# Performance work log

Hardware: AMD Instinct MI355X
Metric: run time of the kernel (lower is better)

Reference implementation:

```python
import jax, jax.numpy as jnp
import numpy as np

S, H, F = 8192, 1024, 15
IN = 1 + F  # scalar target + features per timestep


def _uniform(key, shape, k):
    return jax.random.uniform(key, shape, jnp.float32, -k, k)


def setup_inputs() -> dict:
    key = jax.random.key(0)
    ks = jax.random.split(key, 16)
    k_lstm = 1.0 / np.sqrt(H)  # torch nn.LSTM init scale
    k_ffn = 1.0 / np.sqrt(H)
    return {
        "x": jax.random.normal(ks[0], (S,), jnp.float32),
        "mask": jax.random.randint(ks[1], (S,), 0, 2, jnp.int32),
        "features": jax.random.normal(ks[2], (S, F), jnp.float32),
        "teacher_force_ratio": 1,
        "w_ih0": _uniform(ks[3], (4 * H, IN), k_lstm),
        "w_hh0": _uniform(ks[4], (4 * H, H), k_lstm),
        "b_ih0": _uniform(ks[5], (4 * H,), k_lstm),
        "b_hh0": _uniform(ks[6], (4 * H,), k_lstm),
        "w_ih1": _uniform(ks[7], (4 * H, H), k_lstm),
        "w_hh1": _uniform(ks[8], (4 * H, H), k_lstm),
        "b_ih1": _uniform(ks[9], (4 * H,), k_lstm),
        "b_hh1": _uniform(ks[10], (4 * H,), k_lstm),
        "w_ffn": _uniform(ks[11], (1, H), k_ffn),
        "b_ffn": _uniform(ks[12], (1,), k_ffn),
    }


def _lstm_cell(h, c, inp, w_ih, w_hh, b_ih, b_hh):
    # torch gate order: i, f, g, o
    g = inp @ w_ih.T + h @ w_hh.T + b_ih + b_hh  # (4H,)
    i, f, gg, o = jnp.split(g, 4)
    c_new = jax.nn.sigmoid(f) * c + jax.nn.sigmoid(i) * jnp.tanh(gg)
    h_new = jax.nn.sigmoid(o) * jnp.tanh(c_new)
    return h_new, c_new


def reference(x, mask, features, teacher_force_ratio,
              w_ih0, w_hh0, b_ih0, b_hh0,
              w_ih1, w_hh1, b_ih1, b_hh1,
              w_ffn, b_ffn):
    # teacher_force_ratio==1 => feed x[i] whenever mask[i]!=0 (deterministic).
    # Step 0 always feeds x[0].
    tf = jnp.float32(teacher_force_ratio >= 1)
    use_x = jnp.concatenate([jnp.ones((1,), bool),
                             (mask[1:] != 0) & (tf > 0)])

    def step(carry, inputs):
        h0, c0, h1, c1, prev_y = carry
        xi, sel, fi = inputs
        scalar_in = jnp.where(sel, xi, prev_y)
        inp = jnp.concatenate([scalar_in[None], fi])  # (IN,)
        h0, c0 = _lstm_cell(h0, c0, inp, w_ih0, w_hh0, b_ih0, b_hh0)
        h1, c1 = _lstm_cell(h1, c1, h0, w_ih1, w_hh1, b_ih1, b_hh1)
        y = w_ffn[0] @ h1 + b_ffn[0]  # scalar prediction
        return (h0, c0, h1, c1, y), y

    z = jnp.zeros((H,), x.dtype)
    carry0 = (z, z, z, z, jnp.float32(0.0))
    _, y_hat = jax.lax.scan(step, carry0, (x, use_x, features))
    return y_hat  # (S,)
```

## Files before the change

### kernel.cpp

```cpp
#include <hip/hip_runtime.h>
#include <stdint.h>

typedef float f32x4 __attribute__((ext_vector_type(4)));

#define SLEN 8192
#define NBLK 256

#define RING_PAR 8192
#define H0_OFF   16384
#define WS_BYTES 32768

__device__ __forceinline__ void st_chunk(void* addr, f32x4 v) {
  asm volatile("global_store_dwordx4 %0, %1, off sc0 sc1"
               :: "v"(addr), "v"(v) : "memory");
}
__device__ __forceinline__ f32x4 ld_chunk(const void* a) {
  f32x4 v;
  asm volatile("global_load_dwordx4 %0, %1, off sc0 sc1\n\ts_waitcnt vmcnt(0)"
               : "=v"(v) : "v"(a) : "memory");
  return v;
}
__device__ __forceinline__ void ld2(const void* a, f32x4& v0, f32x4& v1) {
  asm volatile("global_load_dwordx4 %0, %2, off sc0 sc1\n\t"
               "global_load_dwordx4 %1, %2, off offset:16 sc0 sc1\n\t"
               "s_waitcnt vmcnt(0)"
               : "=v"(v0), "=v"(v1) : "v"(a) : "memory");
}
__device__ __forceinline__ void poll2(const void* a, unsigned tag, f32x4& v0, f32x4& v1) {
  ld2(a, v0, v1);
  while (__float_as_uint(v0.w) != tag || __float_as_uint(v1.w) != tag) {
    __builtin_amdgcn_s_sleep(1);
    ld2(a, v0, v1);
  }
}
__device__ __forceinline__ f32x4 poll1(const void* a, unsigned tag) {
  f32x4 v = ld_chunk(a);
  while (__float_as_uint(v.w) != tag) {
    __builtin_amdgcn_s_sleep(1);
    v = ld_chunk(a);
  }
  return v;
}

__device__ __forceinline__ float sigm(float v) { return 1.f / (1.f + expf(-v)); }
__device__ __forceinline__ float tanh_f(float v) {
  float e = expf(-2.f * fabsf(v));
  return copysignf((1.f - e) / (1.f + e), v);
}
__device__ __forceinline__ float lstm_h(float a0, float a1, float a2, float a3, float& c) {
  float ii = sigm(a0), ff = sigm(a1), gg = tanh_f(a2), oo = sigm(a3);
  c = ff * c + ii * gg;
  return oo * tanh_f(c);
}

__device__ __forceinline__ float dpp_red(float x) {
  x += __int_as_float(__builtin_amdgcn_update_dpp(0, __float_as_int(x), 0x111, 0xf, 0xf, true));
  x += __int_as_float(__builtin_amdgcn_update_dpp(0, __float_as_int(x), 0x112, 0xf, 0xf, true));
  x += __int_as_float(__builtin_amdgcn_update_dpp(0, __float_as_int(x), 0x114, 0xf, 0xf, true));
  x += __int_as_float(__builtin_amdgcn_update_dpp(0, __float_as_int(x), 0x118, 0xf, 0xf, true));
  x += __int_as_float(__builtin_amdgcn_update_dpp(0, __float_as_int(x), 0x142, 0xa, 0xf, true));
  x += __int_as_float(__builtin_amdgcn_update_dpp(0, __float_as_int(x), 0x143, 0xc, 0xf, true));
  return x;
}
__device__ __forceinline__ float dot4(f32x4 a, f32x4 b) {
  return a.x * b.x + a.y * b.y + a.z * b.z + a.w * b.w;
}
__device__ __forceinline__ int lds_idx4(int j) { return (j >> 2) * 20 + (j & 3) * 4; }

__global__ __launch_bounds__(512, 2) void lstm_fused(
    const float* __restrict__ x, const int* __restrict__ mask,
    const float* __restrict__ feat, const int* __restrict__ tfp,
    const float* __restrict__ w_ih0, const float* __restrict__ w_hh0,
    const float* __restrict__ b_ih0, const float* __restrict__ b_hh0,
    const float* __restrict__ w_ih1, const float* __restrict__ w_hh1,
    const float* __restrict__ b_ih1, const float* __restrict__ b_hh1,
    const float* __restrict__ w_ffn, const float* __restrict__ b_ffn,
    float* __restrict__ out, char* __restrict__ ws)
{
  char* h1ring = ws;
  char* h0ring = ws + H0_OFF;
  const int tid = threadIdx.x, lane = tid & 63, wv = tid >> 6;
  const int blk = blockIdx.x;
  const int u = wv & 3;
  const int m = blk * 4 + u;
  const bool L1w = wv < 4;

  __shared__ __align__(16) float wh1_lds[16 * 1280];
  __shared__ __align__(16) float lh0[1280];
  __shared__ __align__(16) float lh1[1280];
  __shared__ float lyp[256];
  __shared__ float g1h[4], g1yp[4], g0h[4];
  __shared__ float lys;

  f32x4 W[4][4];
  {
    const float* Wsrc = L1w ? w_ih1 : w_hh0;
#pragma unroll
    for (int g = 0; g < 4; ++g) {
      const f32x4* s = reinterpret_cast<const f32x4*>(
          Wsrc + (size_t)(1024 * g + m) * 1024 + lane * 16);
#pragma unroll
      for (int q = 0; q < 4; ++q) W[g][q] = s[q];
    }
  }
  float wA[4], wB[4];
#pragma unroll
  for (int g = 0; g < 4; ++g) {
    const int r = 1024 * g + m;
    if (L1w) {
      wA[g] = (lane == 16) ? (b_ih1[r] + b_hh1[r]) : 0.f;
      wB[g] = 0.f;
    } else {
      wA[g] = (lane < 16) ? w_ih0[r * 16 + lane]
            : (lane == 16 ? (b_ih0[r] + b_hh0[r]) : 0.f);
      wB[g] = w_ih0[r * 16];
    }
  }
  const float wffn = w_ffn[m];
  const float bf = b_ffn[0];
  float cc = 0.f;

  for (int ch = tid; ch < 1024; ch += 512) {
    const int r = ch >> 6, kc = ch & 63;
    const int grow = 1024 * (r & 3) + blk * 4 + (r >> 2);
    const f32x4* src = reinterpret_cast<const f32x4*>(
        w_hh1 + (size_t)grow * 1024 + kc * 16);
    f32x4* dst = reinterpret_cast<f32x4*>(&wh1_lds[r * 1280 + kc * 20]);
    dst[0] = src[0]; dst[1] = src[1]; dst[2] = src[2]; dst[3] = src[3];
  }
  __syncthreads();

  const bool tf1 = (*tfp) >= 1;

  for (int t = 0; t < SLEN; ++t) {
    const bool use_x = (t == 0) || (tf1 && mask[t] != 0);
    const bool needy = (t > 0) && !use_x;
    float acc0[4];

    if (L1w) {
      if (t > 0) {
        __builtin_amdgcn_s_setprio(1);
        float a[4];
        const f32x4* h0v = reinterpret_cast<const f32x4*>(&lh0[lane * 20]);
        f32x4 p0 = h0v[0], p1 = h0v[1], p2 = h0v[2], p3 = h0v[3];
#pragma unroll
        for (int g = 0; g < 4; ++g)
          a[g] = wA[g] + dot4(W[g][0], p0) + dot4(W[g][1], p1) +
                          dot4(W[g][2], p2) + dot4(W[g][3], p3);
        if (t > 1) {
          const f32x4* h1v = reinterpret_cast<const f32x4*>(&lh1[lane * 20]);
          f32x4 q0 = h1v[0], q1 = h1v[1], q2 = h1v[2], q3 = h1v[3];
#pragma unroll
          for (int g = 0; g < 4; ++g) {
            const f32x4* wb = reinterpret_cast<const f32x4*>(
                &wh1_lds[(u * 4 + g) * 1280 + lane * 20]);
            a[g] += dot4(wb[0], q0) + dot4(wb[1], q1) +
                    dot4(wb[2], q2) + dot4(wb[3], q3);
          }
        }
#pragma unroll
        for (int g = 0; g < 4; ++g) a[g] = dpp_red(a[g]);
        if (lane == 63) {
          float h = lstm_h(a[0], a[1], a[2], a[3], cc);
          g1h[u] = h; g1yp[u] = wffn * h;
        }
        __builtin_amdgcn_s_setprio(0);
      }
    } else {
      float base = (lane == 0) ? (use_x ? x[t] : 0.f)
                 : (lane < 16) ? feat[t * 15 + lane - 1]
                 : (lane == 16) ? 1.f : 0.f;
#pragma unroll
      for (int g = 0; g < 4; ++g) acc0[g] = wA[g] * base;
      if (t > 0) {
        const f32x4* h0v = reinterpret_cast<const f32x4*>(&lh0[lane * 20]);
        f32x4 p0 = h0v[0], p1 = h0v[1], p2 = h0v[2], p3 = h0v[3];
#pragma unroll
        for (int g = 0; g < 4; ++g)
          acc0[g] += dot4(W[g][0], p0) + dot4(W[g][1], p1) +
                     dot4(W[g][2], p2) + dot4(W[g][3], p3);
      }
#pragma unroll
      for (int g = 0; g < 4; ++g) acc0[g] = dpp_red(acc0[g]);
      if (blk == 0 && wv == 4 && t >= 2 && (tf1 && mask[t - 1] != 0)) {
        float s = (lyp[lane * 4] + lyp[lane * 4 + 1]) +
                  (lyp[lane * 4 + 2] + lyp[lane * 4 + 3]);
        s = dpp_red(s);
        if (lane == 63) out[t - 2] = s + bf;
      }
    }
    __syncthreads();

    if (t > 0 && tid < 2) {
      f32x4 v;
      if (tid == 0) { v.x = g1h[0]; v.y = g1h[1]; v.z = g1h[2]; }
      else { v.x = g1h[3]; v.y = (g1yp[0] + g1yp[1]) + (g1yp[2] + g1yp[3]); v.z = 0.f; }
      v.w = __uint_as_float((unsigned)(t - 1));
      st_chunk(h1ring + ((t - 1) & 1) * RING_PAR + blk * 32 + tid * 16, v);
    }
    if (needy) {
      if (tid < 256) {
        f32x4 v = poll1(h1ring + ((t - 1) & 1) * RING_PAR + tid * 32 + 16,
                        (unsigned)(t - 1));
        lyp[tid] = v.y;
      }
      __syncthreads();
      if (wv == 0) {
        float s = (lyp[lane * 4] + lyp[lane * 4 + 1]) +
                  (lyp[lane * 4 + 2] + lyp[lane * 4 + 3]);
        s = dpp_red(s);
        if (lane == 63) {
          float yy = s + bf;
          lys = yy;
          if (blk == 0) out[t - 1] = yy;
        }
      }
      __syncthreads();
    }
    if (!L1w && lane == 63) {
      __builtin_amdgcn_s_setprio(1);
      if (needy) {
        float yy = lys;
#pragma unroll
        for (int g = 0; g < 4; ++g) acc0[g] += yy * wB[g];
      }
      float h = lstm_h(acc0[0], acc0[1], acc0[2], acc0[3], cc);
      g0h[u] = h;
      __builtin_amdgcn_s_setprio(0);
    }
    __syncthreads();

    if (tid < 2) {
      f32x4 v;
      if (tid == 0) { v.x = g0h[0]; v.y = g0h[1]; v.z = g0h[2]; }
      else { v.x = g0h[3]; v.y = 0.f; v.z = 0.f; }
      v.w = __uint_as_float((unsigned)t);
      st_chunk(h0ring + (t & 1) * RING_PAR + blk * 32 + tid * 16, v);
    }
    if (L1w) {
      if (t > 0) {
        f32x4 v0, v1;
        poll2(h1ring + ((t - 1) & 1) * RING_PAR + tid * 32, (unsigned)(t - 1), v0, v1);
        f32x4 hv; hv.x = v0.x; hv.y = v0.y; hv.z = v0.z; hv.w = v1.x;
        *reinterpret_cast<f32x4*>(&lh1[lds_idx4(tid)]) = hv;
        lyp[tid] = v1.y;
      }
    } else {
      const int j = tid - 256;
      f32x4 v0, v1;
      poll2(h0ring + (t & 1) * RING_PAR + j * 32, (unsigned)t, v0, v1);
      f32x4 hv; hv.x = v0.x; hv.y = v0.y; hv.z = v0.z; hv.w = v1.x;
      *reinterpret_cast<f32x4*>(&lh0[lds_idx4(j)]) = hv;
    }
    __syncthreads();
  }

  if (blk == 0 && wv == 4 && (tf1 && mask[SLEN - 1] != 0)) {
    float s = (lyp[lane * 4] + lyp[lane * 4 + 1]) +
              (lyp[lane * 4 + 2] + lyp[lane * 4 + 3]);
    s = dpp_red(s);
    if (lane == 63) out[SLEN - 2] = s + bf;
  }
  if (L1w) {
    float a[4];
    const f32x4* h0v = reinterpret_cast<const f32x4*>(&lh0[lane * 20]);
    f32x4 p0 = h0v[0], p1 = h0v[1], p2 = h0v[2], p3 = h0v[3];
#pragma unroll
    for (int g = 0; g < 4; ++g)
      a[g] = wA[g] + dot4(W[g][0], p0) + dot4(W[g][1], p1) +
                      dot4(W[g][2], p2) + dot4(W[g][3], p3);
    {
      const f32x4* h1v = reinterpret_cast<const f32x4*>(&lh1[lane * 20]);
      f32x4 q0 = h1v[0], q1 = h1v[1], q2 = h1v[2], q3 = h1v[3];
#pragma unroll
      for (int g = 0; g < 4; ++g) {
        const f32x4* wb = reinterpret_cast<const f32x4*>(
            &wh1_lds[(u * 4 + g) * 1280 + lane * 20]);
        a[g] += dot4(wb[0], q0) + dot4(wb[1], q1) +
                dot4(wb[2], q2) + dot4(wb[3], q3);
      }
    }
#pragma unroll
    for (int g = 0; g < 4; ++g) a[g] = dpp_red(a[g]);
    if (lane == 63) {
      float h = lstm_h(a[0], a[1], a[2], a[3], cc);
      g1h[u] = h; g1yp[u] = wffn * h;
    }
  }
  __syncthreads();
  if (tid < 2) {
    f32x4 v;
    if (tid == 0) { v.x = g1h[0]; v.y = g1h[1]; v.z = g1h[2]; }
    else { v.x = g1h[3]; v.y = (g1yp[0] + g1yp[1]) + (g1yp[2] + g1yp[3]); v.z = 0.f; }
    v.w = __uint_as_float((unsigned)(SLEN - 1));
    st_chunk(h1ring + ((SLEN - 1) & 1) * RING_PAR + blk * 32 + tid * 16, v);
    asm volatile("s_waitcnt vmcnt(0)" ::: "memory");
  }
  if (blk == 0) {
    if (tid < 256) {
      f32x4 v = poll1(h1ring + ((SLEN - 1) & 1) * RING_PAR + tid * 32 + 16,
                      (unsigned)(SLEN - 1));
      lyp[tid] = v.y;
    }
    __syncthreads();
    if (wv == 0) {
      float s = (lyp[lane * 4] + lyp[lane * 4 + 1]) +
                (lyp[lane * 4 + 2] + lyp[lane * 4 + 3]);
      s = dpp_red(s);
      if (lane == 63) out[SLEN - 1] = s + bf;
    }
  }
}

extern "C" void kernel_launch(void* const* d_in, const int* in_sizes, int n_in,
                              void* d_out, int out_size, void* d_ws, size_t ws_size,
                              hipStream_t stream) {
  (void)in_sizes; (void)n_in; (void)out_size; (void)ws_size;
  const float* x      = (const float*)d_in[0];
  const int*   mask   = (const int*)  d_in[1];
  const float* feat   = (const float*)d_in[2];
  const int*   tfp    = (const int*)  d_in[3];
  const float* w_ih0  = (const float*)d_in[4];
  const float* w_hh0  = (const float*)d_in[5];
  const float* b_ih0  = (const float*)d_in[6];
  const float* b_hh0  = (const float*)d_in[7];
  const float* w_ih1  = (const float*)d_in[8];
  const float* w_hh1  = (const float*)d_in[9];
  const float* b_ih1  = (const float*)d_in[10];
  const float* b_hh1  = (const float*)d_in[11];
  const float* w_ffn  = (const float*)d_in[12];
  const float* b_ffn  = (const float*)d_in[13];
  float* out = (float*)d_out;
  char*  ws  = (char*)d_ws;

  hipMemsetAsync(d_ws, 0xFF, (size_t)WS_BYTES, stream);

  lstm_fused<<<dim3(NBLK), dim3(512), 0, stream>>>(
      x, mask, feat, tfp, w_ih0, w_hh0, b_ih0, b_hh0,
      w_ih1, w_hh1, b_ih1, b_hh1, w_ffn, b_ffn, out, ws);
}
```

Baseline: 41.07 ms.

## Publish per-unit hidden states directly with tagged 8-byte stores, drop block syncs

Each lane-63 thread now writes its own h value plus step tag as an 8-byte store into a per-unit slot, instead of gathering into shared memory, syncing, and having two threads write 16-byte chunks. This removes two or three __syncthreads per timestep and one LDS round trip on the critical path. The FFN output dot is computed by every block after polling h1 (redundantly), instead of being packed into the ring by producers. Pollers now check four tags per 32-byte read, and the extra redundant polling and FFN work add load on the interconnect.

Measured after the change: 65.79 ms. +60.2%, slower.

```diff
diff --git a/kernel.cpp b/kernel.cpp
--- a/kernel.cpp
+++ b/kernel.cpp
@@ -2,58 +2,48 @@
 #include <stdint.h>
 
 typedef float f32x4 __attribute__((ext_vector_type(4)));
+typedef unsigned int u32x2 __attribute__((ext_vector_type(2)));
 
 #define SLEN 8192
 #define NBLK 256
 
-#define RING_PAR 8192
-#define H0_OFF   16384
+#define H0E_OFF  16384
 #define WS_BYTES 32768
 
-__device__ __forceinline__ void st_chunk(void* addr, f32x4 v) {
-  asm volatile("global_store_dwordx4 %0, %1, off sc0 sc1"
-               :: "v"(addr), "v"(v) : "memory");
-}
-__device__ __forceinline__ f32x4 ld_chunk(const void* a) {
-  f32x4 v;
-  asm volatile("global_load_dwordx4 %0, %1, off sc0 sc1\n\ts_waitcnt vmcnt(0)"
-               : "=v"(v) : "v"(a) : "memory");
-  return v;
-}
-__device__ __forceinline__ void ld2(const void* a, f32x4& v0, f32x4& v1) {
+static __device__ __forceinline__ void st8(void* addr, float h, unsigned tag) {
+  u32x2 e; e.x = __float_as_uint(h); e.y = tag;
+  asm volatile("global_store_dwordx2 %0, %1, off sc0 sc1"
+               :: "v"(addr), "v"(e) : "memory");
+}
+static __device__ __forceinline__ void ld2(const void* a, f32x4& v0, f32x4& v1) {
   asm volatile("global_load_dwordx4 %0, %2, off sc0 sc1\n\t"
                "global_load_dwordx4 %1, %2, off offset:16 sc0 sc1\n\t"
                "s_waitcnt vmcnt(0)"
                : "=v"(v0), "=v"(v1) : "v"(a) : "memory");
 }
-__device__ __forceinline__ void poll2(const void* a, unsigned tag, f32x4& v0, f32x4& v1) {
+static __device__ __forceinline__ void poll_slot(const void* a, unsigned tag,
+                                                 f32x4& v0, f32x4& v1) {
   ld2(a, v0, v1);
-  while (__float_as_uint(v0.w) != tag || __float_as_uint(v1.w) != tag) {
+  while (__float_as_uint(v0.y) != tag || __float_as_uint(v0.w) != tag ||
+         __float_as_uint(v1.y) != tag || __float_as_uint(v1.w) != tag) {
     __builtin_amdgcn_s_sleep(1);
     ld2(a, v0, v1);
   }
 }
-__device__ __forceinline__ f32x4 poll1(const void* a, unsigned tag) {
-  f32x4 v = ld_chunk(a);
-  while (__float_as_uint(v.w) != tag) {
-    __builtin_amdgcn_s_sleep(1);
-    v = ld_chunk(a);
-  }
-  return v;
-}
-
-__device__ __forceinline__ float sigm(float v) { return 1.f / (1.f + expf(-v)); }
-__device__ __forceinline__ float tanh_f(float v) {
+
+static __device__ __forceinline__ float sigm(float v) { return 1.f / (1.f + expf(-v)); }
+static __device__ __forceinline__ float tanh_f(float v) {
   float e = expf(-2.f * fabsf(v));
   return copysignf((1.f - e) / (1.f + e), v);
 }
-__device__ __forceinline__ float lstm_h(float a0, float a1, float a2, float a3, float& c) {
+static __device__ __forceinline__ float lstm_h(float a0, float a1, float a2, float a3,
+                                               float& c) {
   float ii = sigm(a0), ff = sigm(a1), gg = tanh_f(a2), oo = sigm(a3);
   c = ff * c + ii * gg;
   return oo * tanh_f(c);
 }
 
-__device__ __forceinline__ float dpp_red(float x) {
+static __device__ __forceinline__ float dpp_red(float x) {
   x += __int_as_float(__builtin_amdgcn_update_dpp(0, __float_as_int(x), 0x111, 0xf, 0xf, true));
   x += __int_as_float(__builtin_amdgcn_update_dpp(0, __float_as_int(x), 0x112, 0xf, 0xf, true));
   x += __int_as_float(__builtin_amdgcn_update_dpp(0, __float_as_int(x), 0x114, 0xf, 0xf, true));
@@ -62,10 +52,10 @@
   x += __int_as_float(__builtin_amdgcn_update_dpp(0, __float_as_int(x), 0x143, 0xc, 0xf, true));
   return x;
 }
-__device__ __forceinline__ float dot4(f32x4 a, f32x4 b) {
+static __device__ __forceinline__ float dot4(f32x4 a, f32x4 b) {
   return a.x * b.x + a.y * b.y + a.z * b.z + a.w * b.w;
 }
-__device__ __forceinline__ int lds_idx4(int j) { return (j >> 2) * 20 + (j & 3) * 4; }
+static __device__ __forceinline__ int lds_idx4(int j) { return (j >> 2) * 20 + (j & 3) * 4; }
 
 __global__ __launch_bounds__(512, 2) void lstm_fused(
     const float* __restrict__ x, const int* __restrict__ mask,
@@ -77,20 +67,20 @@
     const float* __restrict__ w_ffn, const float* __restrict__ b_ffn,
     float* __restrict__ out, char* __restrict__ ws)
 {
-  char* h1ring = ws;
-  char* h0ring = ws + H0_OFF;
+  char* h1e = ws;
+  char* h0e = ws + H0E_OFF;
   const int tid = threadIdx.x, lane = tid & 63, wv = tid >> 6;
   const int blk = blockIdx.x;
   const int u = wv & 3;
   const int m = blk * 4 + u;
   const bool L1w = wv < 4;
+  const int j = tid & 255;
 
   __shared__ __align__(16) float wh1_lds[16 * 1280];
   __shared__ __align__(16) float lh0[1280];
   __shared__ __align__(16) float lh1[1280];
-  __shared__ float lyp[256];
-  __shared__ float g1h[4], g1yp[4], g0h[4];
-  __shared__ float lys;
+  __shared__ __align__(16) float lyp[256];
+  __shared__ __align__(16) float lypf[256];
 
   f32x4 W[4][4];
   {
@@ -116,7 +106,8 @@
       wB[g] = w_ih0[r * 16];
     }
   }
-  const float wffn = w_ffn[m];
+  const f32x4 wffn4 = L1w ? reinterpret_cast<const f32x4*>(w_ffn)[j]
+                          : f32x4{0.f, 0.f, 0.f, 0.f};
   const float bf = b_ffn[0];
   float cc = 0.f;
 
@@ -131,11 +122,11 @@
   __syncthreads();
 
   const bool tf1 = (*tfp) >= 1;
+  float acc0[4];
 
   for (int t = 0; t < SLEN; ++t) {
     const bool use_x = (t == 0) || (tf1 && mask[t] != 0);
     const bool needy = (t > 0) && !use_x;
-    float acc0[4];
 
     if (L1w) {
       if (t > 0) {
@@ -162,9 +153,21 @@
         for (int g = 0; g < 4; ++g) a[g] = dpp_red(a[g]);
         if (lane == 63) {
           float h = lstm_h(a[0], a[1], a[2], a[3], cc);
-          g1h[u] = h; g1yp[u] = wffn * h;
+          st8(h1e + ((t - 1) & 1) * 8192 + m * 8, h, (unsigned)(t - 1));
         }
         __builtin_amdgcn_s_setprio(0);
+      }
+      if (needy) {
+        f32x4 v0, v1;
+        poll_slot(h1e + ((t - 1) & 1) * 8192 + j * 32, (unsigned)(t - 1), v0, v1);
+        f32x4 h4; h4.x = v0.x; h4.y = v0.z; h4.z = v1.x; h4.w = v1.z;
+        lypf[j] = dot4(wffn4, h4);
+      }
+      if (blk == 0 && wv == 0 && t >= 2) {
+        f32x4 q = reinterpret_cast<const f32x4*>(lyp)[lane];
+        float s = (q.x + q.y) + (q.z + q.w);
+        s = dpp_red(s);
+        if (lane == 63) out[t - 2] = s + bf;
       }
     } else {
       float base = (lane == 0) ? (use_x ? x[t] : 0.f)
@@ -182,85 +185,44 @@
       }
 #pragma unroll
       for (int g = 0; g < 4; ++g) acc0[g] = dpp_red(acc0[g]);
-      if (blk == 0 && wv == 4 && t >= 2 && (tf1 && mask[t - 1] != 0)) {
-        float s = (lyp[lane * 4] + lyp[lane * 4 + 1]) +
-                  (lyp[lane * 4 + 2] + lyp[lane * 4 + 3]);
+    }
+    __syncthreads();
+
+    if (!L1w) {
+      float y = 0.f;
+      if (needy) {
+        f32x4 q = reinterpret_cast<const f32x4*>(lypf)[lane];
+        float s = (q.x + q.y) + (q.z + q.w);
         s = dpp_red(s);
-        if (lane == 63) out[t - 2] = s + bf;
-      }
-    }
-    __syncthreads();
-
-    if (t > 0 && tid < 2) {
-      f32x4 v;
-      if (tid == 0) { v.x = g1h[0]; v.y = g1h[1]; v.z = g1h[2]; }
-      else { v.x = g1h[3]; v.y = (g1yp[0] + g1yp[1]) + (g1yp[2] + g1yp[3]); v.z = 0.f; }
-      v.w = __uint_as_float((unsigned)(t - 1));
-      st_chunk(h1ring + ((t - 1) & 1) * RING_PAR + blk * 32 + tid * 16, v);
-    }
-    if (needy) {
-      if (tid < 256) {
-        f32x4 v = poll1(h1ring + ((t - 1) & 1) * RING_PAR + tid * 32 + 16,
-                        (unsigned)(t - 1));
-        lyp[tid] = v.y;
-      }
-      __syncthreads();
-      if (wv == 0) {
-        float s = (lyp[lane * 4] + lyp[lane * 4 + 1]) +
-                  (lyp[lane * 4 + 2] + lyp[lane * 4 + 3]);
-        s = dpp_red(s);
-        if (lane == 63) {
-          float yy = s + bf;
-          lys = yy;
-          if (blk == 0) out[t - 1] = yy;
+        y = s + bf;
+      }
+      if (lane == 63) {
+        if (needy) {
+#pragma unroll
+          for (int g = 0; g < 4; ++g) acc0[g] += y * wB[g];
         }
-      }
-      __syncthreads();
-    }
-    if (!L1w && lane == 63) {
-      __builtin_amdgcn_s_setprio(1);
-      if (needy) {
-        float yy = lys;
-#pragma unroll
-        for (int g = 0; g < 4; ++g) acc0[g] += yy * wB[g];
-      }
-      float h = lstm_h(acc0[0], acc0[1], acc0[2], acc0[3], cc);
-      g0h[u] = h;
-      __builtin_amdgcn_s_setprio(0);
-    }
-    __syncthreads();
-
-    if (tid < 2) {
-      f32x4 v;
-      if (tid == 0) { v.x = g0h[0]; v.y = g0h[1]; v.z = g0h[2]; }
-      else { v.x = g0h[3]; v.y = 0.f; v.z = 0.f; }
-      v.w = __uint_as_float((unsigned)t);
-      st_chunk(h0ring + (t & 1) * RING_PAR + blk * 32 + tid * 16, v);
-    }
+        float h = lstm_h(acc0[0], acc0[1], acc0[2], acc0[3], cc);
+        st8(h0e + (t & 1) * 8192 + m * 8, h, (unsigned)t);
+      }
+    }
+
     if (L1w) {
       if (t > 0) {
         f32x4 v0, v1;
-        poll2(h1ring + ((t - 1) & 1) * RING_PAR + tid * 32, (unsigned)(t - 1), v0, v1);
-        f32x4 hv; hv.x = v0.x; hv.y = v0.y; hv.z = v0.z; hv.w = v1.x;
-        *reinterpret_cast<f32x4*>(&lh1[lds_idx4(tid)]) = hv;
-        lyp[tid] = v1.y;
+        poll_slot(h1e + ((t - 1) & 1) * 8192 + j * 32, (unsigned)(t - 1), v0, v1);
+        f32x4 h4; h4.x = v0.x; h4.y = v0.z; h4.z = v1.x; h4.w = v1.z;
+        *reinterpret_cast<f32x4*>(&lh1[lds_idx4(j)]) = h4;
+        lyp[j] = dot4(wffn4, h4);
       }
     } else {
-      const int j = tid - 256;
       f32x4 v0, v1;
-      poll2(h0ring + (t & 1) * RING_PAR + j * 32, (unsigned)t, v0, v1);
-      f32x4 hv; hv.x = v0.x; hv.y = v0.y; hv.z = v0.z; hv.w = v1.x;
-      *reinterpret_cast<f32x4*>(&lh0[lds_idx4(j)]) = hv;
+      poll_slot(h0e + (t & 1) * 8192 + j * 32, (unsigned)t, v0, v1);
+      f32x4 h4; h4.x = v0.x; h4.y = v0.z; h4.z = v1.x; h4.w = v1.z;
+      *reinterpret_cast<f32x4*>(&lh0[lds_idx4(j)]) = h4;
     }
     __syncthreads();
   }
 
-  if (blk == 0 && wv == 4 && (tf1 && mask[SLEN - 1] != 0)) {
-    float s = (lyp[lane * 4] + lyp[lane * 4 + 1]) +
-              (lyp[lane * 4 + 2] + lyp[lane * 4 + 3]);
-    s = dpp_red(s);
-    if (lane == 63) out[SLEN - 2] = s + bf;
-  }
   if (L1w) {
     float a[4];
     const f32x4* h0v = reinterpret_cast<const f32x4*>(&lh0[lane * 20]);
@@ -284,28 +246,28 @@
     for (int g = 0; g < 4; ++g) a[g] = dpp_red(a[g]);
     if (lane == 63) {
       float h = lstm_h(a[0], a[1], a[2], a[3], cc);
-      g1h[u] = h; g1yp[u] = wffn * h;
-    }
-  }
-  __syncthreads();
-  if (tid < 2) {
-    f32x4 v;
-    if (tid == 0) { v.x = g1h[0]; v.y = g1h[1]; v.z = g1h[2]; }
-    else { v.x = g1h[3]; v.y = (g1yp[0] + g1yp[1]) + (g1yp[2] + g1yp[3]); v.z = 0.f; }
-    v.w = __uint_as_float((unsigned)(SLEN - 1));
-    st_chunk(h1ring + ((SLEN - 1) & 1) * RING_PAR + blk * 32 + tid * 16, v);
-    asm volatile("s_waitcnt vmcnt(0)" ::: "memory");
-  }
+      st8(h1e + ((SLEN - 1) & 1) * 8192 + m * 8, h, (unsigned)(SLEN - 1));
+    }
+  }
+  asm volatile("s_waitcnt vmcnt(0)" ::: "memory");
+
   if (blk == 0) {
-    if (tid < 256) {
-      f32x4 v = poll1(h1ring + ((SLEN - 1) & 1) * RING_PAR + tid * 32 + 16,
-                      (unsigned)(SLEN - 1));
-      lyp[tid] = v.y;
+    if (wv == 0) {
+      f32x4 q = reinterpret_cast<const f32x4*>(lyp)[lane];
+      float s = (q.x + q.y) + (q.z + q.w);
+      s = dpp_red(s);
+      if (lane == 63) out[SLEN - 2] = s + bf;
+    }
+    if (L1w) {
+      f32x4 v0, v1;
+      poll_slot(h1e + ((SLEN - 1) & 1) * 8192 + j * 32, (unsigned)(SLEN - 1), v0, v1);
+      f32x4 h4; h4.x = v0.x; h4.y = v0.z; h4.z = v1.x; h4.w = v1.z;
+      lypf[j] = dot4(wffn4, h4);
     }
     __syncthreads();
     if (wv == 0) {
-      float s = (lyp[lane * 4] + lyp[lane * 4 + 1]) +
-                (lyp[lane * 4 + 2] + lyp[lane * 4 + 3]);
+      f32x4 q = reinterpret_cast<const f32x4*>(lypf)[lane];
+      float s = (q.x + q.y) + (q.z + q.w);
       s = dpp_red(s);
       if (lane == 63) out[SLEN - 1] = s + bf;
     }
```

## Remove extra block barriers on feedback path and split ring polling across waves

Applied to the files above, without the earlier changes.

The feedback prediction y for non-teacher-forced steps is now computed by each layer-0 wave itself, which polls the h1 ring directly, instead of going through a poll, a syncthreads, a reduction, a second syncthreads and a shared-memory broadcast. The h1 ring reads are duplicated across both wave halves, and each thread now computes the FFN partial from h1 itself. The h0 ring read is split so every thread polls one 16-byte chunk. This is meant to take two block barriers off the serial per-step critical path, at the cost of more redundant global polling traffic.

Result: slower. 51.76 ms (+26.0%).

```diff
diff --git a/kernel.cpp b/kernel.cpp
--- a/kernel.cpp
+++ b/kernel.cpp
@@ -10,50 +10,74 @@
 #define H0_OFF   16384
 #define WS_BYTES 32768
 
-__device__ __forceinline__ void st_chunk(void* addr, f32x4 v) {
+static __device__ __forceinline__ void st_chunk(void* addr, f32x4 v) {
   asm volatile("global_store_dwordx4 %0, %1, off sc0 sc1"
                :: "v"(addr), "v"(v) : "memory");
 }
-__device__ __forceinline__ f32x4 ld_chunk(const void* a) {
+static __device__ __forceinline__ f32x4 ld16(const void* a) {
   f32x4 v;
   asm volatile("global_load_dwordx4 %0, %1, off sc0 sc1\n\ts_waitcnt vmcnt(0)"
                : "=v"(v) : "v"(a) : "memory");
   return v;
 }
-__device__ __forceinline__ void ld2(const void* a, f32x4& v0, f32x4& v1) {
+static __device__ __forceinline__ f32x4 poll16(const void* a, unsigned tag) {
+  f32x4 v = ld16(a);
+  while (__float_as_uint(v.w) != tag) {
+    __builtin_amdgcn_s_sleep(2);
+    v = ld16(a);
+  }
+  return v;
+}
+static __device__ __forceinline__ void ld32(const void* a, f32x4& v0, f32x4& v1) {
   asm volatile("global_load_dwordx4 %0, %2, off sc0 sc1\n\t"
                "global_load_dwordx4 %1, %2, off offset:16 sc0 sc1\n\t"
                "s_waitcnt vmcnt(0)"
                : "=v"(v0), "=v"(v1) : "v"(a) : "memory");
 }
-__device__ __forceinline__ void poll2(const void* a, unsigned tag, f32x4& v0, f32x4& v1) {
-  ld2(a, v0, v1);
+static __device__ __forceinline__ void poll32(const void* a, unsigned tag,
+                                              f32x4& v0, f32x4& v1) {
+  ld32(a, v0, v1);
   while (__float_as_uint(v0.w) != tag || __float_as_uint(v1.w) != tag) {
-    __builtin_amdgcn_s_sleep(1);
-    ld2(a, v0, v1);
-  }
-}
-__device__ __forceinline__ f32x4 poll1(const void* a, unsigned tag) {
-  f32x4 v = ld_chunk(a);
-  while (__float_as_uint(v.w) != tag) {
-    __builtin_amdgcn_s_sleep(1);
-    v = ld_chunk(a);
-  }
-  return v;
-}
-
-__device__ __forceinline__ float sigm(float v) { return 1.f / (1.f + expf(-v)); }
-__device__ __forceinline__ float tanh_f(float v) {
+    __builtin_amdgcn_s_sleep(2);
+    ld32(a, v0, v1);
+  }
+}
+static __device__ __forceinline__ void ld_y4(const char* a0, const char* a1,
+                                             f32x4& v0, f32x4& v1, f32x4& v2, f32x4& v3) {
+  asm volatile("global_load_dwordx4 %0, %4, off sc0 sc1\n\t"
+               "global_load_dwordx4 %1, %4, off offset:2048 sc0 sc1\n\t"
+               "global_load_dwordx4 %2, %5, off sc0 sc1\n\t"
+               "global_load_dwordx4 %3, %5, off offset:2048 sc0 sc1\n\t"
+               "s_waitcnt vmcnt(0)"
+               : "=v"(v0), "=v"(v1), "=v"(v2), "=v"(v3)
+               : "v"(a0), "v"(a1) : "memory");
+}
+static __device__ __forceinline__ float poll_y4(const char* base, int lane, unsigned tag) {
+  const char* a0 = base + lane * 32 + 16;
+  const char* a1 = a0 + 4096;
+  f32x4 v0, v1, v2, v3;
+  ld_y4(a0, a1, v0, v1, v2, v3);
+  while (__float_as_uint(v0.w) != tag || __float_as_uint(v1.w) != tag ||
+         __float_as_uint(v2.w) != tag || __float_as_uint(v3.w) != tag) {
+    __builtin_amdgcn_s_sleep(2);
+    ld_y4(a0, a1, v0, v1, v2, v3);
+  }
+  return (v0.y + v1.y) + (v2.y + v3.y);
+}
+
+static __device__ __forceinline__ float sigm(float v) { return 1.f / (1.f + expf(-v)); }
+static __device__ __forceinline__ float tanh_f(float v) {
   float e = expf(-2.f * fabsf(v));
   return copysignf((1.f - e) / (1.f + e), v);
 }
-__device__ __forceinline__ float lstm_h(float a0, float a1, float a2, float a3, float& c) {
+static __device__ __forceinline__ float lstm_h(float a0, float a1, float a2, float a3,
+                                               float& c) {
   float ii = sigm(a0), ff = sigm(a1), gg = tanh_f(a2), oo = sigm(a3);
   c = ff * c + ii * gg;
   return oo * tanh_f(c);
 }
 
-__device__ __forceinline__ float dpp_red(float x) {
+static __device__ __forceinline__ float dpp_red(float x) {
   x += __int_as_float(__builtin_amdgcn_update_dpp(0, __float_as_int(x), 0x111, 0xf, 0xf, true));
   x += __int_as_float(__builtin_amdgcn_update_dpp(0, __float_as_int(x), 0x112, 0xf, 0xf, true));
   x += __int_as_float(__builtin_amdgcn_update_dpp(0, __float_as_int(x), 0x114, 0xf, 0xf, true));
@@ -62,10 +86,10 @@
   x += __int_as_float(__builtin_amdgcn_update_dpp(0, __float_as_int(x), 0x143, 0xc, 0xf, true));
   return x;
 }
-__device__ __forceinline__ float dot4(f32x4 a, f32x4 b) {
+static __device__ __forceinline__ float dot4(f32x4 a, f32x4 b) {
   return a.x * b.x + a.y * b.y + a.z * b.z + a.w * b.w;
 }
-__device__ __forceinline__ int lds_idx4(int j) { return (j >> 2) * 20 + (j & 3) * 4; }
+static __device__ __forceinline__ int lds_idx4(int j) { return (j >> 2) * 20 + (j & 3) * 4; }
 
 __global__ __launch_bounds__(512, 2) void lstm_fused(
     const float* __restrict__ x, const int* __restrict__ mask,
@@ -88,9 +112,8 @@
   __shared__ __align__(16) float wh1_lds[16 * 1280];
   __shared__ __align__(16) float lh0[1280];
   __shared__ __align__(16) float lh1[1280];
-  __shared__ float lyp[256];
+  __shared__ __align__(16) float lyp[256];
   __shared__ float g1h[4], g1yp[4], g0h[4];
-  __shared__ float lys;
 
   f32x4 W[4][4];
   {
@@ -116,7 +139,9 @@
       wB[g] = w_ih0[r * 16];
     }
   }
-  const float wffn = w_ffn[m];
+  const float wffn_m = w_ffn[m];
+  const f32x4 wffn4 = L1w ? reinterpret_cast<const f32x4*>(w_ffn)[tid & 255]
+                          : f32x4{0.f, 0.f, 0.f, 0.f};
   const float bf = b_ffn[0];
   float cc = 0.f;
 
@@ -131,11 +156,11 @@
   __syncthreads();
 
   const bool tf1 = (*tfp) >= 1;
+  float acc0[4];
 
   for (int t = 0; t < SLEN; ++t) {
     const bool use_x = (t == 0) || (tf1 && mask[t] != 0);
     const bool needy = (t > 0) && !use_x;
-    float acc0[4];
 
     if (L1w) {
       if (t > 0) {
@@ -162,7 +187,7 @@
         for (int g = 0; g < 4; ++g) a[g] = dpp_red(a[g]);
         if (lane == 63) {
           float h = lstm_h(a[0], a[1], a[2], a[3], cc);
-          g1h[u] = h; g1yp[u] = wffn * h;
+          g1h[u] = h; g1yp[u] = wffn_m * h;
         }
         __builtin_amdgcn_s_setprio(0);
       }
@@ -182,9 +207,9 @@
       }
 #pragma unroll
       for (int g = 0; g < 4; ++g) acc0[g] = dpp_red(acc0[g]);
-      if (blk == 0 && wv == 4 && t >= 2 && (tf1 && mask[t - 1] != 0)) {
-        float s = (lyp[lane * 4] + lyp[lane * 4 + 1]) +
-                  (lyp[lane * 4 + 2] + lyp[lane * 4 + 3]);
+      if (blk == 0 && wv == 7 && t >= 2 && (tf1 && mask[t - 1] != 0)) {
+        f32x4 q = reinterpret_cast<const f32x4*>(lyp)[lane];
+        float s = (q.x + q.y) + (q.z + q.w);
         s = dpp_red(s);
         if (lane == 63) out[t - 2] = s + bf;
       }
@@ -198,35 +223,34 @@
       v.w = __uint_as_float((unsigned)(t - 1));
       st_chunk(h1ring + ((t - 1) & 1) * RING_PAR + blk * 32 + tid * 16, v);
     }
-    if (needy) {
-      if (tid < 256) {
-        f32x4 v = poll1(h1ring + ((t - 1) & 1) * RING_PAR + tid * 32 + 16,
-                        (unsigned)(t - 1));
-        lyp[tid] = v.y;
-      }
-      __syncthreads();
-      if (wv == 0) {
-        float s = (lyp[lane * 4] + lyp[lane * 4 + 1]) +
-                  (lyp[lane * 4 + 2] + lyp[lane * 4 + 3]);
+
+    if (L1w) {
+      if (t > 0) {
+        f32x4 v0, v1;
+        poll32(h1ring + ((t - 1) & 1) * RING_PAR + (tid & 255) * 32,
+               (unsigned)(t - 1), v0, v1);
+        f32x4 h4; h4.x = v0.x; h4.y = v0.y; h4.z = v0.z; h4.w = v1.x;
+        *reinterpret_cast<f32x4*>(&lh1[lds_idx4(tid & 255)]) = h4;
+        lyp[tid & 255] = dot4(wffn4, h4);
+      }
+    } else {
+      float y = 0.f;
+      if (needy) {
+        float s = poll_y4(h1ring + ((t - 1) & 1) * RING_PAR, lane, (unsigned)(t - 1));
         s = dpp_red(s);
-        if (lane == 63) {
-          float yy = s + bf;
-          lys = yy;
-          if (blk == 0) out[t - 1] = yy;
+        y = s + bf;
+      }
+      if (lane == 63) {
+        __builtin_amdgcn_s_setprio(1);
+        if (needy) {
+#pragma unroll
+          for (int g = 0; g < 4; ++g) acc0[g] += y * wB[g];
+          if (blk == 0 && wv == 4) out[t - 1] = y;
         }
-      }
-      __syncthreads();
-    }
-    if (!L1w && lane == 63) {
-      __builtin_amdgcn_s_setprio(1);
-      if (needy) {
-        float yy = lys;
-#pragma unroll
-        for (int g = 0; g < 4; ++g) acc0[g] += yy * wB[g];
-      }
-      float h = lstm_h(acc0[0], acc0[1], acc0[2], acc0[3], cc);
-      g0h[u] = h;
-      __builtin_amdgcn_s_setprio(0);
+        float h = lstm_h(acc0[0], acc0[1], acc0[2], acc0[3], cc);
+        g0h[u] = h;
+        __builtin_amdgcn_s_setprio(0);
+      }
     }
     __syncthreads();
 
@@ -237,30 +261,21 @@
       v.w = __uint_as_float((unsigned)t);
       st_chunk(h0ring + (t & 1) * RING_PAR + blk * 32 + tid * 16, v);
     }
-    if (L1w) {
-      if (t > 0) {
-        f32x4 v0, v1;
-        poll2(h1ring + ((t - 1) & 1) * RING_PAR + tid * 32, (unsigned)(t - 1), v0, v1);
-        f32x4 hv; hv.x = v0.x; hv.y = v0.y; hv.z = v0.z; hv.w = v1.x;
-        *reinterpret_cast<f32x4*>(&lh1[lds_idx4(tid)]) = hv;
-        lyp[tid] = v1.y;
-      }
-    } else {
-      const int j = tid - 256;
-      f32x4 v0, v1;
-      poll2(h0ring + (t & 1) * RING_PAR + j * 32, (unsigned)t, v0, v1);
-      f32x4 hv; hv.x = v0.x; hv.y = v0.y; hv.z = v0.z; hv.w = v1.x;
-      *reinterpret_cast<f32x4*>(&lh0[lds_idx4(j)]) = hv;
+
+    {
+      const int j = tid & 255;
+      if (tid < 256) {
+        f32x4 v = poll16(h0ring + (t & 1) * RING_PAR + j * 32, (unsigned)t);
+        const int b = lds_idx4(j);
+        lh0[b + 0] = v.x; lh0[b + 1] = v.y; lh0[b + 2] = v.z;
+      } else {
+        f32x4 v = poll16(h0ring + (t & 1) * RING_PAR + j * 32 + 16, (unsigned)t);
+        lh0[lds_idx4(j) + 3] = v.x;
+      }
     }
     __syncthreads();
   }
 
-  if (blk == 0 && wv == 4 && (tf1 && mask[SLEN - 1] != 0)) {
-    float s = (lyp[lane * 4] + lyp[lane * 4 + 1]) +
-              (lyp[lane * 4 + 2] + lyp[lane * 4 + 3]);
-    s = dpp_red(s);
-    if (lane == 63) out[SLEN - 2] = s + bf;
-  }
   if (L1w) {
     float a[4];
     const f32x4* h0v = reinterpret_cast<const f32x4*>(&lh0[lane * 20]);
@@ -284,8 +299,13 @@
     for (int g = 0; g < 4; ++g) a[g] = dpp_red(a[g]);
     if (lane == 63) {
       float h = lstm_h(a[0], a[1], a[2], a[3], cc);
-      g1h[u] = h; g1yp[u] = wffn * h;
-    }
+      g1h[u] = h; g1yp[u] = wffn_m * h;
+    }
+  } else if (blk == 0 && wv == 7 && (tf1 && mask[SLEN - 1] != 0)) {
+    f32x4 q = reinterpret_cast<const f32x4*>(lyp)[lane];
+    float s = (q.x + q.y) + (q.z + q.w);
+    s = dpp_red(s);
+    if (lane == 63) out[SLEN - 2] = s + bf;
   }
   __syncthreads();
   if (tid < 2) {
@@ -294,21 +314,11 @@
     else { v.x = g1h[3]; v.y = (g1yp[0] + g1yp[1]) + (g1yp[2] + g1yp[3]); v.z = 0.f; }
     v.w = __uint_as_float((unsigned)(SLEN - 1));
     st_chunk(h1ring + ((SLEN - 1) & 1) * RING_PAR + blk * 32 + tid * 16, v);
-    asm volatile("s_waitcnt vmcnt(0)" ::: "memory");
-  }
-  if (blk == 0) {
-    if (tid < 256) {
-      f32x4 v = poll1(h1ring + ((SLEN - 1) & 1) * RING_PAR + tid * 32 + 16,
-                      (unsigned)(SLEN - 1));
-      lyp[tid] = v.y;
-    }
-    __syncthreads();
-    if (wv == 0) {
-      float s = (lyp[lane * 4] + lyp[lane * 4 + 1]) +
-                (lyp[lane * 4 + 2] + lyp[lane * 4 + 3]);
-      s = dpp_red(s);
-      if (lane == 63) out[SLEN - 1] = s + bf;
-    }
+  }
+  if (blk == 0 && wv == 0) {
+    float s = poll_y4(h1ring + ((SLEN - 1) & 1) * RING_PAR, lane, (unsigned)(SLEN - 1));
+    s = dpp_red(s);
+    if (lane == 63) out[SLEN - 1] = s + bf;
   }
 }
 
```
